# Kernel optimization log

Hardware: AMD Instinct MI355X
Metric: run time of the kernel (lower is better)

The kernel has to match this reference:

```python
import jax, jax.numpy as jnp
import numpy as np

N, H, D = 32768, 32, 64


def mobius_addition(x, y, c):
    xy_dot = jnp.sum(x * y, axis=-1, keepdims=True)
    x_norm_sq = jnp.sum(x ** 2, axis=-1, keepdims=True)
    y_norm_sq = jnp.sum(y ** 2, axis=-1, keepdims=True)
    num = (1 + 2 * c * xy_dot + c * y_norm_sq) * x + (1 - c * x_norm_sq) * y
    den = 1 + 2 * c * xy_dot + c * c * x_norm_sq * y_norm_sq
    return num / den


def exp_map(x, v, c):
    v_norm = jnp.linalg.norm(v, axis=-1, keepdims=True)
    sqrt_c = jnp.sqrt(c)
    second = jnp.tanh(sqrt_c * v_norm / 2) * v / (sqrt_c * v_norm)
    return mobius_addition(x, second, c)


def log_map(x, y, c):
    add = mobius_addition(-x, y, c)
    add_norm = jnp.linalg.norm(add, axis=-1, keepdims=True)
    sqrt_c = jnp.sqrt(c)
    return 2 / sqrt_c * jnp.arctanh(sqrt_c * add_norm) * add / add_norm


def setup_inputs() -> dict:
    key = jax.random.key(0)
    ks = jax.random.split(key, 5)
    s = 0.1 / np.sqrt(D)  # keep embeddings well inside the Poincare ball (norm ~0.1)
    return {
        "current_emb": jax.random.normal(ks[0], (N, D), jnp.float32) * s,
        "history": jax.random.normal(ks[1], (H, N, D), jnp.float32) * s,
        "curvature": jnp.ones((1,), jnp.float32),
        "Wq": jax.random.normal(ks[2], (D, D), jnp.float32) / np.sqrt(D),
        "bq": jnp.zeros((D,), jnp.float32),
        "Wk": jax.random.normal(ks[3], (D, D), jnp.float32) / np.sqrt(D),
        "bk": jnp.zeros((D,), jnp.float32),
        "attn_vec": jax.random.normal(ks[4], (D, 1), jnp.float32),
    }


def reference(current_emb, history, curvature, Wq, bq, Wk, bk, attn_vec):
    c = curvature.reshape(())
    origin = jnp.zeros((1, D), current_emb.dtype)
    # log map at origin: hyperbolic -> tangent space
    tangent_current = log_map(origin, current_emb, c)          # [N, D]
    tangent_history = log_map(origin, history, c)              # [H, N, D] (origin broadcasts)
    query = tangent_current @ Wq.T + bq                        # [N, D]
    keys = jnp.einsum('hnd,ed->hne', tangent_history, Wk) + bk  # [H, N, D]
    scores = jnp.tanh(query[None, :, :] + keys)                # [H, N, D]
    weights = scores @ attn_vec                                # [H, N, 1]
    weights = jax.nn.softmax(weights, axis=0)
    weighted_sum = jnp.sum(weights * tangent_history, axis=0)  # [N, D]
    context = exp_map(origin, weighted_sum, c)                 # [N, D]
    return context
```

## Files before the change

### kernel.cpp

```cpp
#include <hip/hip_runtime.h>
#include <math.h>

#define NTOK 32768
#define HH 32
#define DD 64
#define TTOK 32
#define NBLK (NTOK / TTOK)

typedef float f4 __attribute__((ext_vector_type(4)));
typedef short bf16x8 __attribute__((ext_vector_type(8)));

__device__ __forceinline__ float rcpf_(float x) { return __builtin_amdgcn_rcpf(x); }

__device__ __forceinline__ float tanh_f(float x) {
    x = fminf(fmaxf(x, -15.f), 15.f);
    float t = __expf(x + x);
    return (t - 1.f) * rcpf_(t + 1.f);
}

__device__ __forceinline__ float logmap_f(float x) {
    float u = __logf((1.f + x) * rcpf_(1.f - x));
    return (x > 1e-4f) ? u * rcpf_(x) : 2.f;
}

__device__ __forceinline__ bf16x8 hi8(f4 a, f4 b) {
    bf16x8 r;
#pragma unroll
    for (int j = 0; j < 4; ++j) {
        r[j]     = (short)(__float_as_uint(a[j]) >> 16);
        r[j + 4] = (short)(__float_as_uint(b[j]) >> 16);
    }
    return r;
}
__device__ __forceinline__ bf16x8 lo8(f4 a, f4 b) {
    bf16x8 r;
#pragma unroll
    for (int j = 0; j < 4; ++j) {
        float ah = __uint_as_float(__float_as_uint(a[j]) & 0xFFFF0000u);
        float bh = __uint_as_float(__float_as_uint(b[j]) & 0xFFFF0000u);
        r[j]     = (short)(__float_as_uint(a[j] - ah) >> 16);
        r[j + 4] = (short)(__float_as_uint(b[j] - bh) >> 16);
    }
    return r;
}

__device__ __forceinline__ void load_tangent(const float* base, int lane15, int quad,
                                             float sc, f4 yv[8]) {
    const float* rA = base + lane15 * DD + 8 * quad;
    const float* rB = base + (16 + lane15) * DD + 8 * quad;
    yv[0] = *(const f4*)(rA);
    yv[1] = *(const f4*)(rA + 4);
    yv[2] = *(const f4*)(rA + 32);
    yv[3] = *(const f4*)(rA + 36);
    yv[4] = *(const f4*)(rB);
    yv[5] = *(const f4*)(rB + 4);
    yv[6] = *(const f4*)(rB + 32);
    yv[7] = *(const f4*)(rB + 36);
    f4 sA4 = yv[0]*yv[0] + yv[1]*yv[1] + yv[2]*yv[2] + yv[3]*yv[3];
    f4 sB4 = yv[4]*yv[4] + yv[5]*yv[5] + yv[6]*yv[6] + yv[7]*yv[7];
    float nA = sA4[0] + sA4[1] + sA4[2] + sA4[3];
    float nB = sB4[0] + sB4[1] + sB4[2] + sB4[3];
    nA += __shfl_xor(nA, 16); nA += __shfl_xor(nA, 32);
    nB += __shfl_xor(nB, 16); nB += __shfl_xor(nB, 32);
    float fA = logmap_f(sc * sqrtf(nA));
    float fB = logmap_f(sc * sqrtf(nB));
#pragma unroll
    for (int k = 0; k < 4; ++k) { yv[k] = yv[k] * fA; yv[k + 4] = yv[k + 4] * fB; }
}

__device__ __forceinline__ void load_bfrags(const float* W, int lane15, int quad,
                                            bf16x8 Bh[4][2], bf16x8 Bl[4][2]) {
#pragma unroll
    for (int et = 0; et < 4; ++et)
#pragma unroll
        for (int s = 0; s < 2; ++s) {
            const f4* p = (const f4*)(W + (16 * et + lane15) * DD + 32 * s + 8 * quad);
            f4 w0 = p[0], w1 = p[1];
            Bh[et][s] = hi8(w0, w1);
            Bl[et][s] = lo8(w0, w1);
        }
}

__device__ __forceinline__ void mm_accum(const f4 yv[8], const bf16x8 Bh[4][2],
                                         const bf16x8 Bl[4][2], f4 acc[2][4]) {
    bf16x8 Ah[2][2];
#pragma unroll
    for (int tt = 0; tt < 2; ++tt)
#pragma unroll
        for (int s = 0; s < 2; ++s)
            Ah[tt][s] = hi8(yv[tt * 4 + s * 2], yv[tt * 4 + s * 2 + 1]);
#pragma unroll
    for (int tt = 0; tt < 2; ++tt)
#pragma unroll
        for (int s = 0; s < 2; ++s)
#pragma unroll
            for (int et = 0; et < 4; ++et) {
                acc[tt][et] = __builtin_amdgcn_mfma_f32_16x16x32_bf16(Ah[tt][s], Bh[et][s], acc[tt][et], 0, 0, 0);
                acc[tt][et] = __builtin_amdgcn_mfma_f32_16x16x32_bf16(Ah[tt][s], Bl[et][s], acc[tt][et], 0, 0, 0);
            }
    bf16x8 Al[2][2];
#pragma unroll
    for (int tt = 0; tt < 2; ++tt)
#pragma unroll
        for (int s = 0; s < 2; ++s)
            Al[tt][s] = lo8(yv[tt * 4 + s * 2], yv[tt * 4 + s * 2 + 1]);
#pragma unroll
    for (int tt = 0; tt < 2; ++tt)
#pragma unroll
        for (int s = 0; s < 2; ++s)
#pragma unroll
            for (int et = 0; et < 4; ++et)
                acc[tt][et] = __builtin_amdgcn_mfma_f32_16x16x32_bf16(Al[tt][s], Bh[et][s], acc[tt][et], 0, 0, 0);
}

__global__ __launch_bounds__(256, 2) void hyp_attn_mfma(
    const float* __restrict__ cur, const float* __restrict__ hist,
    const float* __restrict__ curv, const float* __restrict__ Wq,
    const float* __restrict__ bq, const float* __restrict__ Wk,
    const float* __restrict__ bk, const float* __restrict__ av,
    float* __restrict__ out)
{
    __shared__ float q2[DD * 36];
    __shared__ float sExch[4][TTOK];
    __shared__ float mBuf[4][TTOK];
    __shared__ float lBuf[4][TTOK];
    __shared__ float oBuf[4][TTOK * 68];

    const int tid    = threadIdx.x;
    const int wv     = tid >> 6;
    const int lane   = tid & 63;
    const int lane15 = lane & 15;
    const int quad   = lane >> 4;
    const int bb     = blockIdx.x;

    const float c  = curv[0];
    const float sc = sqrtf(c);
    const f4 zero4 = {0.f, 0.f, 0.f, 0.f};

    float avC[4];
#pragma unroll
    for (int et = 0; et < 4; ++et) avC[et] = av[16 * et + lane15];

    if (wv == 0) {
        bf16x8 Qh[4][2], Ql[4][2];
        load_bfrags(Wq, lane15, quad, Qh, Ql);
        f4 yv[8];
        load_tangent(cur + (size_t)bb * TTOK * DD, lane15, quad, sc, yv);
        f4 qacc[2][4];
#pragma unroll
        for (int tt = 0; tt < 2; ++tt)
#pragma unroll
            for (int et = 0; et < 4; ++et) qacc[tt][et] = zero4;
        mm_accum(yv, Qh, Ql, qacc);
#pragma unroll
        for (int et = 0; et < 4; ++et) {
            float bias = bq[16 * et + lane15] + bk[16 * et + lane15];
#pragma unroll
            for (int tt = 0; tt < 2; ++tt) {
                f4 qv = qacc[tt][et] + bias;
                *(f4*)&q2[(16 * et + lane15) * 36 + 16 * tt + 4 * quad] = qv;
            }
        }
    }

    bf16x8 Bh[4][2], Bl[4][2];
    load_bfrags(Wk, lane15, quad, Bh, Bl);

    __syncthreads();

    float mA = -3.0e38f, mB = -3.0e38f, lA = 0.f, lB = 0.f;
    f4 OA[4] = {zero4, zero4, zero4, zero4};
    f4 OB[4] = {zero4, zero4, zero4, zero4};

#pragma unroll 1
    for (int i = 0; i < 8; ++i) {
        const int h = wv * 8 + i;
        f4 yv[8];
        load_tangent(hist + ((size_t)h * NTOK + (size_t)bb * TTOK) * DD, lane15, quad, sc, yv);

        f4 acc[2][4];
#pragma unroll
        for (int tt = 0; tt < 2; ++tt)
#pragma unroll
            for (int et = 0; et < 4; ++et) acc[tt][et] = zero4;
        mm_accum(yv, Bh, Bl, acc);

        f4 sv0 = zero4, sv1 = zero4;
#pragma unroll
        for (int et = 0; et < 4; ++et)
#pragma unroll
            for (int tt = 0; tt < 2; ++tt) {
                f4 qv = *(const f4*)&q2[(16 * et + lane15) * 36 + 16 * tt + 4 * quad];
                f4 x = acc[tt][et] + qv;
                f4 tn;
#pragma unroll
                for (int r = 0; r < 4; ++r) tn[r] = tanh_f(x[r]);
                if (tt == 0) sv0 += tn * avC[et]; else sv1 += tn * avC[et];
            }
#pragma unroll
        for (int st = 1; st < 16; st <<= 1)
#pragma unroll
            for (int r = 0; r < 4; ++r) {
                sv0[r] += __shfl_xor(sv0[r], st);
                sv1[r] += __shfl_xor(sv1[r], st);
            }
        if (lane15 == 0) {
#pragma unroll
            for (int r = 0; r < 4; ++r) {
                sExch[wv][4 * quad + r]      = sv0[r];
                sExch[wv][16 + 4 * quad + r] = sv1[r];
            }
        }
        float sA = sExch[wv][lane15];
        float sB = sExch[wv][16 + lane15];

        float mAn = fmaxf(mA, sA), mBn = fmaxf(mB, sB);
        float aA = __expf(mA - mAn), pA = __expf(sA - mAn);
        float aB = __expf(mB - mBn), pB = __expf(sB - mBn);
        lA = lA * aA + pA; mA = mAn;
        lB = lB * aB + pB; mB = mBn;
#pragma unroll
        for (int k = 0; k < 4; ++k) {
            OA[k] = OA[k] * aA + yv[k] * pA;
            OB[k] = OB[k] * aB + yv[k + 4] * pB;
        }
    }

    if (quad == 0) {
        mBuf[wv][lane15] = mA; mBuf[wv][16 + lane15] = mB;
        lBuf[wv][lane15] = lA; lBuf[wv][16 + lane15] = lB;
    }
    __syncthreads();
    float MA = fmaxf(fmaxf(mBuf[0][lane15], mBuf[1][lane15]),
                     fmaxf(mBuf[2][lane15], mBuf[3][lane15]));
    float MB = fmaxf(fmaxf(mBuf[0][16 + lane15], mBuf[1][16 + lane15]),
                     fmaxf(mBuf[2][16 + lane15], mBuf[3][16 + lane15]));
    float bA = __expf(mA - MA), bB = __expf(mB - MB);
#pragma unroll
    for (int k = 0; k < 4; ++k) { OA[k] = OA[k] * bA; OB[k] = OB[k] * bB; }
    {
        float* oA = &oBuf[wv][lane15 * 68];
        float* oB = &oBuf[wv][(16 + lane15) * 68];
        *(f4*)(oA + 8 * quad)      = OA[0];
        *(f4*)(oA + 8 * quad + 4)  = OA[1];
        *(f4*)(oA + 32 + 8 * quad) = OA[2];
        *(f4*)(oA + 36 + 8 * quad) = OA[3];
        *(f4*)(oB + 8 * quad)      = OB[0];
        *(f4*)(oB + 8 * quad + 4)  = OB[1];
        *(f4*)(oB + 32 + 8 * quad) = OB[2];
        *(f4*)(oB + 36 + 8 * quad) = OB[3];
    }
    __syncthreads();

    {
        const int tok = tid >> 3;
        const int d0  = (tid & 7) * 8;
        f4 o0 = zero4, o1 = zero4;
#pragma unroll
        for (int w = 0; w < 4; ++w) {
            o0 += *(const f4*)&oBuf[w][tok * 68 + d0];
            o1 += *(const f4*)&oBuf[w][tok * 68 + d0 + 4];
        }
        float M = fmaxf(fmaxf(mBuf[0][tok], mBuf[1][tok]),
                        fmaxf(mBuf[2][tok], mBuf[3][tok]));
        float L = lBuf[0][tok] * __expf(mBuf[0][tok] - M)
                + lBuf[1][tok] * __expf(mBuf[1][tok] - M)
                + lBuf[2][tok] * __expf(mBuf[2][tok] - M)
                + lBuf[3][tok] * __expf(mBuf[3][tok] - M);
        float rl = rcpf_(L);
        o0 = o0 * rl; o1 = o1 * rl;
        f4 sq = o0 * o0 + o1 * o1;
        float nv = sq[0] + sq[1] + sq[2] + sq[3];
        nv += __shfl_xor(nv, 1); nv += __shfl_xor(nv, 2); nv += __shfl_xor(nv, 4);
        float x = sc * sqrtf(nv);
        float g = (x > 1e-4f) ? tanh_f(0.5f * x) * rcpf_(x) : 0.5f;
        float* op = out + ((size_t)bb * TTOK + tok) * DD + d0;
        *(f4*)(op)     = o0 * g;
        *(f4*)(op + 4) = o1 * g;
    }
}

extern "C" void kernel_launch(void* const* d_in, const int* in_sizes, int n_in,
                              void* d_out, int out_size, void* d_ws, size_t ws_size,
                              hipStream_t stream) {
    const float* cur  = (const float*)d_in[0];
    const float* hist = (const float*)d_in[1];
    const float* curv = (const float*)d_in[2];
    const float* Wq   = (const float*)d_in[3];
    const float* bq   = (const float*)d_in[4];
    const float* Wk   = (const float*)d_in[5];
    const float* bk   = (const float*)d_in[6];
    const float* av   = (const float*)d_in[7];
    float* out = (float*)d_out;

    hipLaunchKernelGGL(hyp_attn_mfma, dim3(NBLK), dim3(256), 0, stream,
                       cur, hist, curv, Wq, bq, Wk, bk, av, out);
}
```

Baseline: 392.0 us.

## Split work per wave into 16-token halves with double-buffered history prefetch

Each wave now handles 16 tokens over 16 history steps instead of 32 tokens over 8 steps, and two waves split the history for each token group. The query is computed redundantly per wave in registers rather than shared through LDS. The next history tile is prefetched into a second register buffer so load latency overlaps compute. The output accumulator lives in LDS to cut register pressure, allowing 3 blocks per CU instead of 2, at the cost of extra LDS traffic every step.

```diff
diff --git a/kernel.cpp b/kernel.cpp
--- a/kernel.cpp
+++ b/kernel.cpp
@@ -4,8 +4,8 @@
 #define NTOK 32768
 #define HH 32
 #define DD 64
-#define TTOK 32
-#define NBLK (NTOK / TTOK)
+#define TPB 32
+#define NBLK (NTOK / TPB)
 
 typedef float f4 __attribute__((ext_vector_type(4)));
 typedef short bf16x8 __attribute__((ext_vector_type(8)));
@@ -44,239 +44,198 @@
     return r;
 }
 
-__device__ __forceinline__ void load_tangent(const float* base, int lane15, int quad,
-                                             float sc, f4 yv[8]) {
-    const float* rA = base + lane15 * DD + 8 * quad;
-    const float* rB = base + (16 + lane15) * DD + 8 * quad;
-    yv[0] = *(const f4*)(rA);
-    yv[1] = *(const f4*)(rA + 4);
-    yv[2] = *(const f4*)(rA + 32);
-    yv[3] = *(const f4*)(rA + 36);
-    yv[4] = *(const f4*)(rB);
-    yv[5] = *(const f4*)(rB + 4);
-    yv[6] = *(const f4*)(rB + 32);
-    yv[7] = *(const f4*)(rB + 36);
-    f4 sA4 = yv[0]*yv[0] + yv[1]*yv[1] + yv[2]*yv[2] + yv[3]*yv[3];
-    f4 sB4 = yv[4]*yv[4] + yv[5]*yv[5] + yv[6]*yv[6] + yv[7]*yv[7];
-    float nA = sA4[0] + sA4[1] + sA4[2] + sA4[3];
-    float nB = sB4[0] + sB4[1] + sB4[2] + sB4[3];
-    nA += __shfl_xor(nA, 16); nA += __shfl_xor(nA, 32);
-    nB += __shfl_xor(nB, 16); nB += __shfl_xor(nB, 32);
-    float fA = logmap_f(sc * sqrtf(nA));
-    float fB = logmap_f(sc * sqrtf(nB));
-#pragma unroll
-    for (int k = 0; k < 4; ++k) { yv[k] = yv[k] * fA; yv[k + 4] = yv[k + 4] * fB; }
-}
-
-__device__ __forceinline__ void load_bfrags(const float* W, int lane15, int quad,
+__device__ __forceinline__ void load_bfrags(const float* W, int l15, int quad,
                                             bf16x8 Bh[4][2], bf16x8 Bl[4][2]) {
 #pragma unroll
     for (int et = 0; et < 4; ++et)
 #pragma unroll
         for (int s = 0; s < 2; ++s) {
-            const f4* p = (const f4*)(W + (16 * et + lane15) * DD + 32 * s + 8 * quad);
+            const f4* p = (const f4*)(W + (16 * et + l15) * DD + 32 * s + 8 * quad);
             f4 w0 = p[0], w1 = p[1];
             Bh[et][s] = hi8(w0, w1);
             Bl[et][s] = lo8(w0, w1);
         }
 }
 
-__device__ __forceinline__ void mm_accum(const f4 yv[8], const bf16x8 Bh[4][2],
-                                         const bf16x8 Bl[4][2], f4 acc[2][4]) {
-    bf16x8 Ah[2][2];
-#pragma unroll
-    for (int tt = 0; tt < 2; ++tt)
-#pragma unroll
-        for (int s = 0; s < 2; ++s)
-            Ah[tt][s] = hi8(yv[tt * 4 + s * 2], yv[tt * 4 + s * 2 + 1]);
-#pragma unroll
-    for (int tt = 0; tt < 2; ++tt)
-#pragma unroll
-        for (int s = 0; s < 2; ++s)
-#pragma unroll
-            for (int et = 0; et < 4; ++et) {
-                acc[tt][et] = __builtin_amdgcn_mfma_f32_16x16x32_bf16(Ah[tt][s], Bh[et][s], acc[tt][et], 0, 0, 0);
-                acc[tt][et] = __builtin_amdgcn_mfma_f32_16x16x32_bf16(Ah[tt][s], Bl[et][s], acc[tt][et], 0, 0, 0);
-            }
-    bf16x8 Al[2][2];
-#pragma unroll
-    for (int tt = 0; tt < 2; ++tt)
-#pragma unroll
-        for (int s = 0; s < 2; ++s)
-            Al[tt][s] = lo8(yv[tt * 4 + s * 2], yv[tt * 4 + s * 2 + 1]);
-#pragma unroll
-    for (int tt = 0; tt < 2; ++tt)
-#pragma unroll
-        for (int s = 0; s < 2; ++s)
-#pragma unroll
-            for (int et = 0; et < 4; ++et)
-                acc[tt][et] = __builtin_amdgcn_mfma_f32_16x16x32_bf16(Al[tt][s], Bh[et][s], acc[tt][et], 0, 0, 0);
-}
-
-__global__ __launch_bounds__(256, 2) void hyp_attn_mfma(
+__device__ __forceinline__ void load4(const float* base, int l15, int quad, f4 yv[4]) {
+    const float* r = base + l15 * DD + 8 * quad;
+    yv[0] = *(const f4*)(r);
+    yv[1] = *(const f4*)(r + 4);
+    yv[2] = *(const f4*)(r + 32);
+    yv[3] = *(const f4*)(r + 36);
+}
+
+__device__ __forceinline__ void tangent_scale(f4 yv[4], float sc) {
+    f4 s4 = yv[0]*yv[0] + yv[1]*yv[1] + yv[2]*yv[2] + yv[3]*yv[3];
+    float n = s4[0] + s4[1] + s4[2] + s4[3];
+    n += __shfl_xor(n, 16);
+    n += __shfl_xor(n, 32);
+    float f = logmap_f(sc * sqrtf(n));
+#pragma unroll
+    for (int k = 0; k < 4; ++k) yv[k] = yv[k] * f;
+}
+
+__device__ __forceinline__ void mm16(const f4 yv[4], const bf16x8 Bh[4][2],
+                                     const bf16x8 Bl[4][2], f4 acc[4]) {
+    bf16x8 Ah0 = hi8(yv[0], yv[1]);
+    bf16x8 Ah1 = hi8(yv[2], yv[3]);
+#pragma unroll
+    for (int et = 0; et < 4; ++et) {
+        acc[et] = __builtin_amdgcn_mfma_f32_16x16x32_bf16(Ah0, Bh[et][0], acc[et], 0, 0, 0);
+        acc[et] = __builtin_amdgcn_mfma_f32_16x16x32_bf16(Ah1, Bh[et][1], acc[et], 0, 0, 0);
+        acc[et] = __builtin_amdgcn_mfma_f32_16x16x32_bf16(Ah0, Bl[et][0], acc[et], 0, 0, 0);
+        acc[et] = __builtin_amdgcn_mfma_f32_16x16x32_bf16(Ah1, Bl[et][1], acc[et], 0, 0, 0);
+    }
+    bf16x8 Al0 = lo8(yv[0], yv[1]);
+    bf16x8 Al1 = lo8(yv[2], yv[3]);
+#pragma unroll
+    for (int et = 0; et < 4; ++et) {
+        acc[et] = __builtin_amdgcn_mfma_f32_16x16x32_bf16(Al0, Bh[et][0], acc[et], 0, 0, 0);
+        acc[et] = __builtin_amdgcn_mfma_f32_16x16x32_bf16(Al1, Bh[et][1], acc[et], 0, 0, 0);
+    }
+}
+
+__global__ __launch_bounds__(256, 3) void hyp_attn_v3(
     const float* __restrict__ cur, const float* __restrict__ hist,
     const float* __restrict__ curv, const float* __restrict__ Wq,
     const float* __restrict__ bq, const float* __restrict__ Wk,
     const float* __restrict__ bk, const float* __restrict__ av,
     float* __restrict__ out)
 {
-    __shared__ float q2[DD * 36];
-    __shared__ float sExch[4][TTOK];
-    __shared__ float mBuf[4][TTOK];
-    __shared__ float lBuf[4][TTOK];
-    __shared__ float oBuf[4][TTOK * 68];
-
-    const int tid    = threadIdx.x;
-    const int wv     = tid >> 6;
-    const int lane   = tid & 63;
-    const int lane15 = lane & 15;
-    const int quad   = lane >> 4;
-    const int bb     = blockIdx.x;
-
-    const float c  = curv[0];
-    const float sc = sqrtf(c);
+    __shared__ float oBuf[4][16][68];
+    __shared__ float sEx[4][16];
+    __shared__ float mBuf[4][16];
+    __shared__ float lBuf[4][16];
+
+    const int tid  = threadIdx.x;
+    const int wv   = tid >> 6;
+    const int lane = tid & 63;
+    const int l15  = lane & 15;
+    const int quad = lane >> 4;
+    const int pair = wv >> 1;
+    const int sub  = wv & 1;
+    const int bb   = blockIdx.x;
+    const int tok0 = bb * TPB + pair * 16;
+
+    const float sc = sqrtf(curv[0]);
     const f4 zero4 = {0.f, 0.f, 0.f, 0.f};
 
     float avC[4];
 #pragma unroll
-    for (int et = 0; et < 4; ++et) avC[et] = av[16 * et + lane15];
-
-    if (wv == 0) {
+    for (int et = 0; et < 4; ++et) avC[et] = av[16 * et + l15];
+
+    f4 qC[4] = {zero4, zero4, zero4, zero4};
+    {
         bf16x8 Qh[4][2], Ql[4][2];
-        load_bfrags(Wq, lane15, quad, Qh, Ql);
-        f4 yv[8];
-        load_tangent(cur + (size_t)bb * TTOK * DD, lane15, quad, sc, yv);
-        f4 qacc[2][4];
-#pragma unroll
-        for (int tt = 0; tt < 2; ++tt)
-#pragma unroll
-            for (int et = 0; et < 4; ++et) qacc[tt][et] = zero4;
-        mm_accum(yv, Qh, Ql, qacc);
+        load_bfrags(Wq, l15, quad, Qh, Ql);
+        f4 yv[4];
+        load4(cur + (size_t)tok0 * DD, l15, quad, yv);
+        tangent_scale(yv, sc);
+        mm16(yv, Qh, Ql, qC);
+#pragma unroll
+        for (int et = 0; et < 4; ++et)
+            qC[et] += bq[16 * et + l15] + bk[16 * et + l15];
+    }
+
+    bf16x8 Bh[4][2], Bl[4][2];
+    load_bfrags(Wk, l15, quad, Bh, Bl);
+
+    float* oP = &oBuf[wv][l15][0];
+    *(f4*)(oP + 8 * quad)      = zero4;
+    *(f4*)(oP + 8 * quad + 4)  = zero4;
+    *(f4*)(oP + 32 + 8 * quad) = zero4;
+    *(f4*)(oP + 36 + 8 * quad) = zero4;
+
+    const size_t hstep = (size_t)NTOK * DD;
+    const float* hb = hist + ((size_t)(sub * 16) * NTOK + tok0) * DD;
+
+    float m = -3.0e38f, l = 0.f;
+    f4 yb[2][4];
+    load4(hb, l15, quad, yb[0]);
+
+#pragma unroll 2
+    for (int i = 0; i < 16; ++i) {
+        f4* cv = yb[i & 1];
+        if (i + 1 < 16)
+            load4(hb + (size_t)(i + 1) * hstep, l15, quad, yb[(i + 1) & 1]);
+
+        tangent_scale(cv, sc);
+
+        f4 acc[4] = {zero4, zero4, zero4, zero4};
+        mm16(cv, Bh, Bl, acc);
+
+        f4 sv = zero4;
 #pragma unroll
         for (int et = 0; et < 4; ++et) {
-            float bias = bq[16 * et + lane15] + bk[16 * et + lane15];
-#pragma unroll
-            for (int tt = 0; tt < 2; ++tt) {
-                f4 qv = qacc[tt][et] + bias;
-                *(f4*)&q2[(16 * et + lane15) * 36 + 16 * tt + 4 * quad] = qv;
-            }
+            f4 x = acc[et] + qC[et];
+            f4 tn;
+#pragma unroll
+            for (int r = 0; r < 4; ++r) tn[r] = tanh_f(x[r]);
+            sv += tn * avC[et];
         }
-    }
-
-    bf16x8 Bh[4][2], Bl[4][2];
-    load_bfrags(Wk, lane15, quad, Bh, Bl);
-
+#pragma unroll
+        for (int st = 1; st < 16; st <<= 1)
+#pragma unroll
+            for (int r = 0; r < 4; ++r) sv[r] += __shfl_xor(sv[r], st);
+
+        if (l15 == 0) {
+#pragma unroll
+            for (int r = 0; r < 4; ++r) sEx[wv][4 * quad + r] = sv[r];
+        }
+        float s = sEx[wv][l15];
+
+        float mn = fmaxf(m, s);
+        float a  = __expf(m - mn);
+        float p  = __expf(s - mn);
+        l = l * a + p;
+        m = mn;
+
+        f4 o0 = *(const f4*)(oP + 8 * quad);
+        f4 o1 = *(const f4*)(oP + 8 * quad + 4);
+        f4 o2 = *(const f4*)(oP + 32 + 8 * quad);
+        f4 o3 = *(const f4*)(oP + 36 + 8 * quad);
+        o0 = o0 * a + cv[0] * p;
+        o1 = o1 * a + cv[1] * p;
+        o2 = o2 * a + cv[2] * p;
+        o3 = o3 * a + cv[3] * p;
+        *(f4*)(oP + 8 * quad)      = o0;
+        *(f4*)(oP + 8 * quad + 4)  = o1;
+        *(f4*)(oP + 32 + 8 * quad) = o2;
+        *(f4*)(oP + 36 + 8 * quad) = o3;
+    }
+
+    if (quad == 0) { mBuf[wv][l15] = m; lBuf[wv][l15] = l; }
     __syncthreads();
 
-    float mA = -3.0e38f, mB = -3.0e38f, lA = 0.f, lB = 0.f;
-    f4 OA[4] = {zero4, zero4, zero4, zero4};
-    f4 OB[4] = {zero4, zero4, zero4, zero4};
-
-#pragma unroll 1
-    for (int i = 0; i < 8; ++i) {
-        const int h = wv * 8 + i;
-        f4 yv[8];
-        load_tangent(hist + ((size_t)h * NTOK + (size_t)bb * TTOK) * DD, lane15, quad, sc, yv);
-
-        f4 acc[2][4];
-#pragma unroll
-        for (int tt = 0; tt < 2; ++tt)
-#pragma unroll
-            for (int et = 0; et < 4; ++et) acc[tt][et] = zero4;
-        mm_accum(yv, Bh, Bl, acc);
-
-        f4 sv0 = zero4, sv1 = zero4;
-#pragma unroll
-        for (int et = 0; et < 4; ++et)
-#pragma unroll
-            for (int tt = 0; tt < 2; ++tt) {
-                f4 qv = *(const f4*)&q2[(16 * et + lane15) * 36 + 16 * tt + 4 * quad];
-                f4 x = acc[tt][et] + qv;
-                f4 tn;
-#pragma unroll
-                for (int r = 0; r < 4; ++r) tn[r] = tanh_f(x[r]);
-                if (tt == 0) sv0 += tn * avC[et]; else sv1 += tn * avC[et];
-            }
-#pragma unroll
-        for (int st = 1; st < 16; st <<= 1)
-#pragma unroll
-            for (int r = 0; r < 4; ++r) {
-                sv0[r] += __shfl_xor(sv0[r], st);
-                sv1[r] += __shfl_xor(sv1[r], st);
-            }
-        if (lane15 == 0) {
-#pragma unroll
-            for (int r = 0; r < 4; ++r) {
-                sExch[wv][4 * quad + r]      = sv0[r];
-                sExch[wv][16 + 4 * quad + r] = sv1[r];
-            }
-        }
-        float sA = sExch[wv][lane15];
-        float sB = sExch[wv][16 + lane15];
-
-        float mAn = fmaxf(mA, sA), mBn = fmaxf(mB, sB);
-        float aA = __expf(mA - mAn), pA = __expf(sA - mAn);
-        float aB = __expf(mB - mBn), pB = __expf(sB - mBn);
-        lA = lA * aA + pA; mA = mAn;
-        lB = lB * aB + pB; mB = mBn;
-#pragma unroll
-        for (int k = 0; k < 4; ++k) {
-            OA[k] = OA[k] * aA + yv[k] * pA;
-            OB[k] = OB[k] * aB + yv[k + 4] * pB;
-        }
-    }
-
-    if (quad == 0) {
-        mBuf[wv][lane15] = mA; mBuf[wv][16 + lane15] = mB;
-        lBuf[wv][lane15] = lA; lBuf[wv][16 + lane15] = lB;
-    }
-    __syncthreads();
-    float MA = fmaxf(fmaxf(mBuf[0][lane15], mBuf[1][lane15]),
-                     fmaxf(mBuf[2][lane15], mBuf[3][lane15]));
-    float MB = fmaxf(fmaxf(mBuf[0][16 + lane15], mBuf[1][16 + lane15]),
-                     fmaxf(mBuf[2][16 + lane15], mBuf[3][16 + lane15]));
-    float bA = __expf(mA - MA), bB = __expf(mB - MB);
-#pragma unroll
-    for (int k = 0; k < 4; ++k) { OA[k] = OA[k] * bA; OB[k] = OB[k] * bB; }
-    {
-        float* oA = &oBuf[wv][lane15 * 68];
-        float* oB = &oBuf[wv][(16 + lane15) * 68];
-        *(f4*)(oA + 8 * quad)      = OA[0];
-        *(f4*)(oA + 8 * quad + 4)  = OA[1];
-        *(f4*)(oA + 32 + 8 * quad) = OA[2];
-        *(f4*)(oA + 36 + 8 * quad) = OA[3];
-        *(f4*)(oB + 8 * quad)      = OB[0];
-        *(f4*)(oB + 8 * quad + 4)  = OB[1];
-        *(f4*)(oB + 32 + 8 * quad) = OB[2];
-        *(f4*)(oB + 36 + 8 * quad) = OB[3];
-    }
-    __syncthreads();
-
-    {
-        const int tok = tid >> 3;
-        const int d0  = (tid & 7) * 8;
-        f4 o0 = zero4, o1 = zero4;
-#pragma unroll
-        for (int w = 0; w < 4; ++w) {
-            o0 += *(const f4*)&oBuf[w][tok * 68 + d0];
-            o1 += *(const f4*)&oBuf[w][tok * 68 + d0 + 4];
-        }
-        float M = fmaxf(fmaxf(mBuf[0][tok], mBuf[1][tok]),
-                        fmaxf(mBuf[2][tok], mBuf[3][tok]));
-        float L = lBuf[0][tok] * __expf(mBuf[0][tok] - M)
-                + lBuf[1][tok] * __expf(mBuf[1][tok] - M)
-                + lBuf[2][tok] * __expf(mBuf[2][tok] - M)
-                + lBuf[3][tok] * __expf(mBuf[3][tok] - M);
+    if (sub == 0) {
+        const int w0 = 2 * pair, w1 = 2 * pair + 1;
+        float m0 = mBuf[w0][l15], m1 = mBuf[w1][l15];
+        float l0 = lBuf[w0][l15], l1 = lBuf[w1][l15];
+        float M  = fmaxf(m0, m1);
+        float a0 = __expf(m0 - M), a1 = __expf(m1 - M);
+        float L  = l0 * a0 + l1 * a1;
         float rl = rcpf_(L);
-        o0 = o0 * rl; o1 = o1 * rl;
-        f4 sq = o0 * o0 + o1 * o1;
+
+        const float* p0 = &oBuf[w0][l15][0];
+        const float* p1 = &oBuf[w1][l15][0];
+        f4 o0 = (*(const f4*)(p0 + 8 * quad))      * a0 + (*(const f4*)(p1 + 8 * quad))      * a1;
+        f4 o1 = (*(const f4*)(p0 + 8 * quad + 4))  * a0 + (*(const f4*)(p1 + 8 * quad + 4))  * a1;
+        f4 o2 = (*(const f4*)(p0 + 32 + 8 * quad)) * a0 + (*(const f4*)(p1 + 32 + 8 * quad)) * a1;
+        f4 o3 = (*(const f4*)(p0 + 36 + 8 * quad)) * a0 + (*(const f4*)(p1 + 36 + 8 * quad)) * a1;
+        o0 = o0 * rl; o1 = o1 * rl; o2 = o2 * rl; o3 = o3 * rl;
+
+        f4 sq = o0 * o0 + o1 * o1 + o2 * o2 + o3 * o3;
         float nv = sq[0] + sq[1] + sq[2] + sq[3];
-        nv += __shfl_xor(nv, 1); nv += __shfl_xor(nv, 2); nv += __shfl_xor(nv, 4);
+        nv += __shfl_xor(nv, 16);
+        nv += __shfl_xor(nv, 32);
         float x = sc * sqrtf(nv);
         float g = (x > 1e-4f) ? tanh_f(0.5f * x) * rcpf_(x) : 0.5f;
-        float* op = out + ((size_t)bb * TTOK + tok) * DD + d0;
-        *(f4*)(op)     = o0 * g;
-        *(f4*)(op + 4) = o1 * g;
+
+        float* op = out + (size_t)(tok0 + l15) * DD + 8 * quad;
+        *(f4*)(op)      = o0 * g;
+        *(f4*)(op + 4)  = o1 * g;
+        *(f4*)(op + 32) = o2 * g;
+        *(f4*)(op + 36) = o3 * g;
     }
 }
 
@@ -293,6 +252,6 @@
     const float* av   = (const float*)d_in[7];
     float* out = (float*)d_out;
 
-    hipLaunchKernelGGL(hyp_attn_mfma, dim3(NBLK), dim3(256), 0, stream,
+    hipLaunchKernelGGL(hyp_attn_v3, dim3(NBLK), dim3(256), 0, stream,
                        cur, hist, curv, Wq, bq, Wk, bk, av, out);
 }
```

Result: slower. 534.2 us (+36.3%).
